# Kernel tuning notes

Hardware: AMD Instinct MI355X
Metric: run time of the kernel (lower is better)

The kernel has to match this reference:

```python
import jax, jax.numpy as jnp
import numpy as np

N, IN_F, OUT_F = 65536, 512, 512


def setup_inputs() -> dict:
    key = jax.random.key(0)
    k1, k2, k3 = jax.random.split(key, 3)
    # Activations arrive as dequant-pending uint8-valued floats in [0, 256).
    x = jax.random.randint(k1, (N, IN_F), 0, 256).astype(jnp.float32)
    weight = jax.random.randint(k2, (OUT_F, IN_F), 0, 256).astype(jnp.int32)
    bias = jax.random.randint(k3, (OUT_F,), -512, 512).astype(jnp.int32)
    return {
        "x": x,
        "weight": weight,
        "bias": bias,
        "M": jnp.asarray(0.0123, dtype=jnp.float32),
        "x_zero": jnp.asarray(128.0, dtype=jnp.float32),
        "w_zero": jnp.asarray(128.0, dtype=jnp.float32),
        "y_zero": jnp.asarray(128.0, dtype=jnp.float32),
    }


def reference(x, weight, bias, M, x_zero, w_zero, y_zero):
    # y = round(linear(x - x_zero, w - w_zero, b) * M + y_zero)
    xs = x - x_zero                                   # [N, IN_F]
    w = weight.astype(jnp.float32) - w_zero           # [OUT_F, IN_F]
    y = jnp.einsum("ni,oi->no", xs, w) + bias.astype(jnp.float32)
    return jnp.round(y * M + y_zero)
```

## Files before the change

### kernel.cpp

```cpp
#include <hip/hip_runtime.h>
#include <hip/hip_bf16.h>


#define K_DIM 512
#define OUTF  512
#define BM    128
#define BN    128
#define BK    64
#define NT    8
#define LDA   72
#define AB_ELE (128 * LDA)

typedef __attribute__((ext_vector_type(8))) short bf16x8;
typedef __attribute__((ext_vector_type(4))) float f32x4;
typedef __attribute__((ext_vector_type(4))) unsigned short u16x4;
typedef __attribute__((ext_vector_type(4))) unsigned int u32x4;
typedef __attribute__((ext_vector_type(4))) int i32x4;

__device__ __forceinline__ unsigned short f2bf(float f) {
    union { float f; unsigned int u; } v; v.f = f;
    unsigned int u = v.u + 0x7fffu + ((v.u >> 16) & 1u);
    return (unsigned short)(u >> 16);
}

__global__ void wprep_kernel(const int* __restrict__ W,
                             unsigned short* __restrict__ Wb,
                             const float* __restrict__ wzp) {
    float wz = wzp[0];
    int idx = (blockIdx.x * blockDim.x + threadIdx.x) * 4;
    i32x4 w = *reinterpret_cast<const i32x4*>(W + idx);
    u16x4 h;
    h[0] = f2bf((float)w[0] - wz);
    h[1] = f2bf((float)w[1] - wz);
    h[2] = f2bf((float)w[2] - wz);
    h[3] = f2bf((float)w[3] - wz);
    *reinterpret_cast<u16x4*>(Wb + idx) = h;
}

__global__ __launch_bounds__(256, 2)
void qlinear_gemm(const float* __restrict__ X,
                  const unsigned short* __restrict__ Wb,
                  const int* __restrict__ bias,
                  const float* __restrict__ Mp,
                  const float* __restrict__ xzp,
                  const float* __restrict__ yzp,
                  float* __restrict__ Y) {
    __shared__ unsigned short lds[4 * AB_ELE];
    const int BOF = 2 * AB_ELE;

    const int tid = threadIdx.x;
    const int lane = tid & 63;
    const int wid = tid >> 6;
    const int wr = wid >> 1, wc = wid & 1;
    const int fr = lane & 15, fq = lane >> 4;

    const int b = blockIdx.x;
    const int lid = (b & 7) * 256 + (b >> 3);
    const int rowTile = lid >> 2, colTile = lid & 3;
    const int row0 = rowTile * BM;
    const int n0 = colTile * BN;

    const float xz = xzp[0];

    const float* xbase = X + (size_t)(row0 + (tid >> 4)) * K_DIM + (tid & 15) * 4;
    const unsigned short* wbase = Wb + (size_t)(n0 + (tid >> 3)) * K_DIM + (tid & 7) * 8;
    const int awoff = (tid >> 4) * LDA + (tid & 15) * 4;
    const int bwoff = BOF + (tid >> 3) * LDA + (tid & 7) * 8;

    f32x4 ra[8];
    u32x4 rb[4];

    auto loadTile = [&](int t) {
        const float* xp = xbase + t * BK;
        #pragma unroll
        for (int i = 0; i < 8; ++i)
            ra[i] = *reinterpret_cast<const f32x4*>(xp + (size_t)i * 16 * K_DIM);
        const unsigned short* wp = wbase + t * BK;
        #pragma unroll
        for (int i = 0; i < 4; ++i)
            rb[i] = *reinterpret_cast<const u32x4*>(wp + (size_t)i * 32 * K_DIM);
    };
    auto writeTile = [&](int buf) {
        const int ab = buf * AB_ELE;
        #pragma unroll
        for (int i = 0; i < 8; ++i) {
            u16x4 h;
            h[0] = f2bf(ra[i][0] - xz);
            h[1] = f2bf(ra[i][1] - xz);
            h[2] = f2bf(ra[i][2] - xz);
            h[3] = f2bf(ra[i][3] - xz);
            *reinterpret_cast<u16x4*>(&lds[ab + awoff + i * 16 * LDA]) = h;
        }
        #pragma unroll
        for (int i = 0; i < 4; ++i)
            *reinterpret_cast<u32x4*>(&lds[ab + bwoff + i * 32 * LDA]) = rb[i];
    };

    f32x4 acc[4][4] = {};

    const int aro = (wr * 64 + fr) * LDA + fq * 8;
    const int bro = BOF + (wc * 64 + fr) * LDA + fq * 8;

    auto computeTile = [&](int buf) {
        const int ab = buf * AB_ELE;
        #pragma unroll
        for (int ks = 0; ks < 2; ++ks) {
            bf16x8 af[4], bfr[4];
            #pragma unroll
            for (int m = 0; m < 4; ++m)
                af[m] = *reinterpret_cast<const bf16x8*>(&lds[ab + aro + m * 16 * LDA + ks * 32]);
            #pragma unroll
            for (int n = 0; n < 4; ++n)
                bfr[n] = *reinterpret_cast<const bf16x8*>(&lds[ab + bro + n * 16 * LDA + ks * 32]);
            #pragma unroll
            for (int m = 0; m < 4; ++m)
                #pragma unroll
                for (int n = 0; n < 4; ++n)
                    acc[m][n] = __builtin_amdgcn_mfma_f32_16x16x32_bf16(
                        af[m], bfr[n], acc[m][n], 0, 0, 0);
        }
    };

    loadTile(0);
    writeTile(0);
    __syncthreads();

    #pragma unroll
    for (int t = 0; t < NT; ++t) {
        if (t < NT - 1) loadTile(t + 1);
        computeTile(t & 1);
        if (t < NT - 1) writeTile((t + 1) & 1);
        __syncthreads();
    }

    const float M = Mp[0], yz = yzp[0];
    #pragma unroll
    for (int n = 0; n < 4; ++n) {
        const int col = n0 + wc * 64 + n * 16 + fr;
        const float bv = (float)bias[col];
        #pragma unroll
        for (int m = 0; m < 4; ++m) {
            const int row = row0 + wr * 64 + m * 16 + fq * 4;
            float* yp = Y + (size_t)row * OUTF + col;
            #pragma unroll
            for (int j = 0; j < 4; ++j)
                yp[(size_t)j * OUTF] = rintf((acc[m][n][j] + bv) * M + yz);
        }
    }
}

extern "C" void kernel_launch(void* const* d_in, const int* in_sizes, int n_in,
                              void* d_out, int out_size, void* d_ws, size_t ws_size,
                              hipStream_t stream) {
    const float* x    = (const float*)d_in[0];
    const int*   w    = (const int*)d_in[1];
    const int*   bias = (const int*)d_in[2];
    const float* M    = (const float*)d_in[3];
    const float* xz   = (const float*)d_in[4];
    const float* wz   = (const float*)d_in[5];
    const float* yz   = (const float*)d_in[6];
    float* y = (float*)d_out;
    unsigned short* Wb = (unsigned short*)d_ws;

    wprep_kernel<<<256, 256, 0, stream>>>(w, Wb, wz);
    qlinear_gemm<<<2048, 256, 0, stream>>>(x, Wb, bias, M, xz, yz, y);
}
```

Baseline: 79.76 us.

## Switch quantized GEMM from bf16 MFMA to exact int8 MFMA

Activations and weights are now zero-point shifted and packed as int8 instead of bf16, and the GEMM uses the i32 16x16x64 int8 MFMA with integer accumulation and integer bias add. This halves LDS footprint and traffic per tile and doubles MFMA throughput per instruction. Blocks grow to 512 threads with a 2x4 wave layout and a padded 80-byte LDS row stride. It relies on inputs lying in the uint8 range, which the task states; values outside it would wrap.

```diff
diff --git a/kernel.cpp b/kernel.cpp
--- a/kernel.cpp
+++ b/kernel.cpp
@@ -1,5 +1,4 @@
 #include <hip/hip_runtime.h>
-#include <hip/hip_bf16.h>
 
 
 #define K_DIM 512
@@ -8,143 +7,127 @@
 #define BN    128
 #define BK    64
 #define NT    8
-#define LDA   72
-#define AB_ELE (128 * LDA)
+#define LDAB  80
+#define TILE_B (128 * LDAB)
+#define BUF_B  (2 * TILE_B)
 
-typedef __attribute__((ext_vector_type(8))) short bf16x8;
+typedef __attribute__((ext_vector_type(4))) int i32x4;
 typedef __attribute__((ext_vector_type(4))) float f32x4;
-typedef __attribute__((ext_vector_type(4))) unsigned short u16x4;
-typedef __attribute__((ext_vector_type(4))) unsigned int u32x4;
-typedef __attribute__((ext_vector_type(4))) int i32x4;
 
-__device__ __forceinline__ unsigned short f2bf(float f) {
-    union { float f; unsigned int u; } v; v.f = f;
-    unsigned int u = v.u + 0x7fffu + ((v.u >> 16) & 1u);
-    return (unsigned short)(u >> 16);
+__device__ __forceinline__ unsigned int pack4(float a, float b, float c, float d, float z) {
+    unsigned int b0 = (unsigned int)((int)(a - z)) & 0xffu;
+    unsigned int b1 = (unsigned int)((int)(b - z)) & 0xffu;
+    unsigned int b2 = (unsigned int)((int)(c - z)) & 0xffu;
+    unsigned int b3 = (unsigned int)((int)(d - z)) & 0xffu;
+    return b0 | (b1 << 8) | (b2 << 16) | (b3 << 24);
 }
 
-__global__ void wprep_kernel(const int* __restrict__ W,
-                             unsigned short* __restrict__ Wb,
-                             const float* __restrict__ wzp) {
+__global__ void wprep(const int* __restrict__ W, unsigned int* __restrict__ Wb,
+                      const float* __restrict__ wzp) {
     float wz = wzp[0];
     int idx = (blockIdx.x * blockDim.x + threadIdx.x) * 4;
     i32x4 w = *reinterpret_cast<const i32x4*>(W + idx);
-    u16x4 h;
-    h[0] = f2bf((float)w[0] - wz);
-    h[1] = f2bf((float)w[1] - wz);
-    h[2] = f2bf((float)w[2] - wz);
-    h[3] = f2bf((float)w[3] - wz);
-    *reinterpret_cast<u16x4*>(Wb + idx) = h;
+    Wb[idx >> 2] = pack4((float)w[0], (float)w[1], (float)w[2], (float)w[3], wz);
 }
 
-__global__ __launch_bounds__(256, 2)
-void qlinear_gemm(const float* __restrict__ X,
-                  const unsigned short* __restrict__ Wb,
-                  const int* __restrict__ bias,
-                  const float* __restrict__ Mp,
-                  const float* __restrict__ xzp,
-                  const float* __restrict__ yzp,
-                  float* __restrict__ Y) {
-    __shared__ unsigned short lds[4 * AB_ELE];
-    const int BOF = 2 * AB_ELE;
+__global__ __launch_bounds__(512, 4)
+void qgemm(const float* __restrict__ X,
+           const unsigned char* __restrict__ Wb,
+           const int* __restrict__ bias,
+           const float* __restrict__ Mp,
+           const float* __restrict__ xzp,
+           const float* __restrict__ yzp,
+           float* __restrict__ Y) {
+    __shared__ unsigned char lds[2 * BUF_B];
 
-    const int tid = threadIdx.x;
+    const int tid  = threadIdx.x;
     const int lane = tid & 63;
-    const int wid = tid >> 6;
-    const int wr = wid >> 1, wc = wid & 1;
-    const int fr = lane & 15, fq = lane >> 4;
+    const int wid  = tid >> 6;
+    const int wr   = wid >> 2;
+    const int wc   = wid & 3;
+    const int fr   = lane & 15;
+    const int fq   = lane >> 4;
 
     const int b = blockIdx.x;
     const int lid = (b & 7) * 256 + (b >> 3);
-    const int rowTile = lid >> 2, colTile = lid & 3;
-    const int row0 = rowTile * BM;
-    const int n0 = colTile * BN;
+    const int row0 = (lid >> 2) * BM;
+    const int n0   = (lid & 3) * BN;
 
     const float xz = xzp[0];
 
-    const float* xbase = X + (size_t)(row0 + (tid >> 4)) * K_DIM + (tid & 15) * 4;
-    const unsigned short* wbase = Wb + (size_t)(n0 + (tid >> 3)) * K_DIM + (tid & 7) * 8;
-    const int awoff = (tid >> 4) * LDA + (tid & 15) * 4;
-    const int bwoff = BOF + (tid >> 3) * LDA + (tid & 7) * 8;
+    const int srow = tid >> 2;
+    const int scol = (tid & 3) * 16;
+    const float* xbase = X + (size_t)(row0 + srow) * K_DIM + scol;
+    const unsigned char* wbase = Wb + (size_t)(n0 + srow) * K_DIM + scol;
+    const int aoff = srow * LDAB + scol;
+    const int boff = TILE_B + srow * LDAB + scol;
 
-    f32x4 ra[8];
-    u32x4 rb[4];
+    f32x4 ra[4];
+    i32x4 rb;
 
-    auto loadTile = [&](int t) {
+    auto stage = [&](int t) {
         const float* xp = xbase + t * BK;
         #pragma unroll
-        for (int i = 0; i < 8; ++i)
-            ra[i] = *reinterpret_cast<const f32x4*>(xp + (size_t)i * 16 * K_DIM);
-        const unsigned short* wp = wbase + t * BK;
+        for (int q = 0; q < 4; ++q)
+            ra[q] = *reinterpret_cast<const f32x4*>(xp + q * 4);
+        rb = *reinterpret_cast<const i32x4*>(wbase + t * BK);
+    };
+    auto convwrite = [&](int buf) {
+        const int ab = buf * BUF_B;
+        i32x4 pa;
         #pragma unroll
-        for (int i = 0; i < 4; ++i)
-            rb[i] = *reinterpret_cast<const u32x4*>(wp + (size_t)i * 32 * K_DIM);
-    };
-    auto writeTile = [&](int buf) {
-        const int ab = buf * AB_ELE;
-        #pragma unroll
-        for (int i = 0; i < 8; ++i) {
-            u16x4 h;
-            h[0] = f2bf(ra[i][0] - xz);
-            h[1] = f2bf(ra[i][1] - xz);
-            h[2] = f2bf(ra[i][2] - xz);
-            h[3] = f2bf(ra[i][3] - xz);
-            *reinterpret_cast<u16x4*>(&lds[ab + awoff + i * 16 * LDA]) = h;
-        }
-        #pragma unroll
-        for (int i = 0; i < 4; ++i)
-            *reinterpret_cast<u32x4*>(&lds[ab + bwoff + i * 32 * LDA]) = rb[i];
+        for (int q = 0; q < 4; ++q)
+            pa[q] = (int)pack4(ra[q][0], ra[q][1], ra[q][2], ra[q][3], xz);
+        *reinterpret_cast<i32x4*>(&lds[ab + aoff]) = pa;
+        *reinterpret_cast<i32x4*>(&lds[ab + boff]) = rb;
     };
 
-    f32x4 acc[4][4] = {};
+    i32x4 acc[4][2] = {};
 
-    const int aro = (wr * 64 + fr) * LDA + fq * 8;
-    const int bro = BOF + (wc * 64 + fr) * LDA + fq * 8;
+    const int aro = (wr * 64 + fr) * LDAB + fq * 16;
+    const int bro = TILE_B + (wc * 32 + fr) * LDAB + fq * 16;
 
-    auto computeTile = [&](int buf) {
-        const int ab = buf * AB_ELE;
+    auto compute = [&](int buf) {
+        const int ab = buf * BUF_B;
+        i32x4 af[4], bf[2];
         #pragma unroll
-        for (int ks = 0; ks < 2; ++ks) {
-            bf16x8 af[4], bfr[4];
+        for (int m = 0; m < 4; ++m)
+            af[m] = *reinterpret_cast<const i32x4*>(&lds[ab + aro + m * 16 * LDAB]);
+        #pragma unroll
+        for (int n = 0; n < 2; ++n)
+            bf[n] = *reinterpret_cast<const i32x4*>(&lds[ab + bro + n * 16 * LDAB]);
+        #pragma unroll
+        for (int m = 0; m < 4; ++m)
             #pragma unroll
-            for (int m = 0; m < 4; ++m)
-                af[m] = *reinterpret_cast<const bf16x8*>(&lds[ab + aro + m * 16 * LDA + ks * 32]);
-            #pragma unroll
-            for (int n = 0; n < 4; ++n)
-                bfr[n] = *reinterpret_cast<const bf16x8*>(&lds[ab + bro + n * 16 * LDA + ks * 32]);
-            #pragma unroll
-            for (int m = 0; m < 4; ++m)
-                #pragma unroll
-                for (int n = 0; n < 4; ++n)
-                    acc[m][n] = __builtin_amdgcn_mfma_f32_16x16x32_bf16(
-                        af[m], bfr[n], acc[m][n], 0, 0, 0);
-        }
+            for (int n = 0; n < 2; ++n)
+                acc[m][n] = __builtin_amdgcn_mfma_i32_16x16x64_i8(
+                    af[m], bf[n], acc[m][n], 0, 0, 0);
     };
 
-    loadTile(0);
-    writeTile(0);
+    stage(0);
+    convwrite(0);
     __syncthreads();
 
     #pragma unroll
     for (int t = 0; t < NT; ++t) {
-        if (t < NT - 1) loadTile(t + 1);
-        computeTile(t & 1);
-        if (t < NT - 1) writeTile((t + 1) & 1);
+        if (t < NT - 1) stage(t + 1);
+        compute(t & 1);
+        if (t < NT - 1) convwrite((t + 1) & 1);
         __syncthreads();
     }
 
     const float M = Mp[0], yz = yzp[0];
     #pragma unroll
-    for (int n = 0; n < 4; ++n) {
-        const int col = n0 + wc * 64 + n * 16 + fr;
-        const float bv = (float)bias[col];
+    for (int n = 0; n < 2; ++n) {
+        const int col = n0 + wc * 32 + n * 16 + fr;
+        const int bv = bias[col];
         #pragma unroll
         for (int m = 0; m < 4; ++m) {
             const int row = row0 + wr * 64 + m * 16 + fq * 4;
             float* yp = Y + (size_t)row * OUTF + col;
             #pragma unroll
             for (int j = 0; j < 4; ++j)
-                yp[(size_t)j * OUTF] = rintf((acc[m][n][j] + bv) * M + yz);
+                yp[(size_t)j * OUTF] = rintf((float)(acc[m][n][j] + bv) * M + yz);
         }
     }
 }
@@ -160,8 +143,8 @@
     const float* wz   = (const float*)d_in[5];
     const float* yz   = (const float*)d_in[6];
     float* y = (float*)d_out;
-    unsigned short* Wb = (unsigned short*)d_ws;
+    unsigned int* Wb = (unsigned int*)d_ws;
 
-    wprep_kernel<<<256, 256, 0, stream>>>(w, Wb, wz);
-    qlinear_gemm<<<2048, 256, 0, stream>>>(x, Wb, bias, M, xz, yz, y);
+    wprep<<<256, 256, 0, stream>>>(w, Wb, wz);
+    qgemm<<<2048, 512, 0, stream>>>(x, (const unsigned char*)Wb, bias, M, xz, yz, y);
 }
```

After: 76.54 us. -4.0%, faster.
